# Performance work log

Hardware: AMD Instinct MI355X
Metric: run time of the kernel (lower is better)

Reference implementation:

```python
import jax, jax.numpy as jnp
import numpy as np

D_MODEL = 1024
NHEAD = 16
HEAD_DIM = D_MODEL // NHEAD
B, T = 4, 2048


def setup_inputs() -> dict:
    key = jax.random.key(0)
    ks = jax.random.split(key, 5)
    s = 0.02
    return {
        "x": jax.random.normal(ks[0], (B, T, D_MODEL), dtype=jnp.float32),
        "w_qkv": jax.random.normal(ks[1], (D_MODEL, 3 * D_MODEL), dtype=jnp.float32) * s,
        "b_qkv": jnp.zeros((3 * D_MODEL,), dtype=jnp.float32),
        "w_proj": jax.random.normal(ks[2], (D_MODEL, D_MODEL), dtype=jnp.float32) * s,
        "b_proj": jnp.zeros((D_MODEL,), dtype=jnp.float32),
    }


def reference(x, w_qkv, b_qkv, w_proj, b_proj):
    Bx, Tx, D = x.shape
    qkv = x @ w_qkv + b_qkv                      # [B,T,3D]
    qkv = qkv.reshape(Bx, Tx, 3, NHEAD, HEAD_DIM)
    q, k, v = qkv[:, :, 0], qkv[:, :, 1], qkv[:, :, 2]   # [B,T,H,hd]
    q = q.transpose(0, 2, 1, 3)                  # [B,H,T,hd]
    k = k.transpose(0, 2, 1, 3)
    v = v.transpose(0, 2, 1, 3)
    scale = 1.0 / jnp.sqrt(jnp.asarray(HEAD_DIM, dtype=x.dtype))
    attn = jnp.einsum("bhqd,bhkd->bhqk", q, k) * scale   # [B,H,T,T]
    causal = jnp.tril(jnp.ones((Tx, Tx), dtype=bool))
    attn = jnp.where(causal[None, None], attn, jnp.asarray(-jnp.inf, dtype=attn.dtype))
    attn = jax.nn.softmax(attn, axis=-1)
    # dropout p=0.0 (eval / identity)
    out = jnp.einsum("bhqk,bhkd->bhqd", attn, v)          # [B,H,T,hd]
    out = out.transpose(0, 2, 1, 3).reshape(Bx, Tx, D)
    return out @ w_proj + b_proj
```

## Files before the change

### kernel.cpp

```cpp
#include <hip/hip_runtime.h>
#include <hip/hip_bf16.h>
#include <math.h>

#define D_MODEL 1024
#define NH      16
#define HD      64
#define T_SEQ   2048
#define B_SZ    4
#define M_ROWS  (B_SZ * T_SEQ)
#define N_QKV   (3 * D_MODEL)

typedef __bf16 bf16x8 __attribute__((ext_vector_type(8)));
typedef __bf16 bf16x4 __attribute__((ext_vector_type(4)));
typedef float  f32x4  __attribute__((ext_vector_type(4)));

__device__ __forceinline__ bf16x8 cvt8(float4 a, float4 b) {
    bf16x8 v;
    v[0]=(__bf16)a.x; v[1]=(__bf16)a.y; v[2]=(__bf16)a.z; v[3]=(__bf16)a.w;
    v[4]=(__bf16)b.x; v[5]=(__bf16)b.y; v[6]=(__bf16)b.z; v[7]=(__bf16)b.w;
    return v;
}

__device__ __forceinline__ void gload_lds16(const __bf16* g, __bf16* l) {
    __builtin_amdgcn_global_load_lds(
        (const __attribute__((address_space(1))) void*)g,
        (__attribute__((address_space(3))) void*)l, 16, 0, 0);
}

__global__ __launch_bounds__(256) void cvt_bf16(const float* __restrict__ in,
                                                __bf16* __restrict__ out, int n8)
{
    int i = blockIdx.x * 256 + threadIdx.x;
    if (i < n8) {
        float4 a = ((const float4*)in)[2 * i];
        float4 b = ((const float4*)in)[2 * i + 1];
        ((bf16x8*)out)[i] = cvt8(a, b);
    }
}

__global__ __launch_bounds__(256) void transpose_cvt(
    const float* __restrict__ W, __bf16* __restrict__ WT, int R, int C)
{
    __shared__ float t[32][33];
    const int tr0 = blockIdx.y * 32, tc0 = blockIdx.x * 32;
    const int lr = threadIdx.x >> 5, lc = threadIdx.x & 31;
    #pragma unroll
    for (int i = 0; i < 4; ++i)
        t[lr + i * 8][lc] = W[(size_t)(tr0 + lr + i * 8) * C + tc0 + lc];
    __syncthreads();
    #pragma unroll
    for (int i = 0; i < 4; ++i)
        WT[(size_t)(tc0 + lr + i * 8) * R + tr0 + lc] = (__bf16)t[lc][lr + i * 8];
}

template<int MODE>
__global__ __launch_bounds__(256) void gemm_mfma(
    const __bf16* __restrict__ A, const __bf16* __restrict__ BT,
    const float* __restrict__ bias, void* __restrict__ C0,
    __bf16* __restrict__ vT, int M, int N, int K)
{
    __shared__ __bf16 As[128 * 32];
    __shared__ __bf16 Bs[128 * 32];

    const int nbn = N >> 7;
    const int nwg = gridDim.x;
    int bid = blockIdx.x;
    bid = (bid & 7) * (nwg >> 3) + (bid >> 3);
    const int tm = bid / nbn, tn = bid % nbn;
    const int row0 = tm << 7, col0 = tn << 7;

    const int tid  = threadIdx.x;
    const int wid  = tid >> 6, lane = tid & 63;
    const int wm   = wid >> 1, wn = wid & 1;
    const int g    = lane >> 4, r16 = lane & 15;

    const int srow = lane >> 2;
    const int skk  = (lane & 3) * 8;

    f32x4 acc[4][4] = {};

    for (int k0 = 0; k0 < K; k0 += 32) {
        #pragma unroll
        for (int i = 0; i < 2; ++i) {
            const int seg = wid * 2 + i;
            const int row = seg * 16 + srow;
            gload_lds16(A  + (size_t)(row0 + row) * K + k0 + skk, As + seg * 512);
            gload_lds16(BT + (size_t)(col0 + row) * K + k0 + skk, Bs + seg * 512);
        }
        __syncthreads();

        bf16x8 af[4], bfr[4];
        #pragma unroll
        for (int mt = 0; mt < 4; ++mt)
            af[mt] = *(const bf16x8*)&As[(wm * 64 + mt * 16 + r16) * 32 + g * 8];
        #pragma unroll
        for (int nt = 0; nt < 4; ++nt)
            bfr[nt] = *(const bf16x8*)&Bs[(wn * 64 + nt * 16 + r16) * 32 + g * 8];
        #pragma unroll
        for (int mt = 0; mt < 4; ++mt)
            #pragma unroll
            for (int nt = 0; nt < 4; ++nt)
                acc[mt][nt] = __builtin_amdgcn_mfma_f32_16x16x32_bf16(
                    af[mt], bfr[nt], acc[mt][nt], 0, 0, 0);
        __syncthreads();
    }

    const bool isV = (MODE == 1) && (tn >= 16);

    #pragma unroll
    for (int mt = 0; mt < 4; ++mt) {
        #pragma unroll
        for (int nt = 0; nt < 4; ++nt) {
            const int col = col0 + wn * 64 + nt * 16 + r16;
            const float bv = bias[col];
            const int rowb = row0 + wm * 64 + mt * 16 + g * 4;
            if (MODE == 0) {
                #pragma unroll
                for (int j = 0; j < 4; ++j)
                    ((float*)C0)[(size_t)(rowb + j) * N + col] = acc[mt][nt][j] + bv;
            } else if (!isV) {
                #pragma unroll
                for (int j = 0; j < 4; ++j)
                    ((__bf16*)C0)[(size_t)(rowb + j) * 2048 + col] =
                        (__bf16)(acc[mt][nt][j] + bv);
            } else {
                const int hh = (col - 2048) >> 6, dd = (col - 2048) & 63;
                const int bb = rowb >> 11, tt = rowb & 2047;
                __bf16 p4[4];
                #pragma unroll
                for (int j = 0; j < 4; ++j) p4[j] = (__bf16)(acc[mt][nt][j] + bv);
                *(bf16x4*)&vT[((size_t)((bb * NH + hh) * HD + dd)) * T_SEQ + tt]
                    = *(const bf16x4*)p4;
            }
        }
    }
}

__global__ __launch_bounds__(256) void attn_mfma(
    const __bf16* __restrict__ qkb, const __bf16* __restrict__ vT,
    __bf16* __restrict__ aout)
{
    const int idx = blockIdx.x;
    const int qt  = 15 - (idx >> 6);
    const int bh  = idx & 63;
    const int b   = bh >> 4;
    const int h   = bh & 15;
    const int tid  = threadIdx.x;
    const int wid  = tid >> 6;
    const int lane = tid & 63;
    const int g    = lane >> 4;
    const int n    = lane & 15;
    const int swzn = (n & 7) << 4;

    const int q0    = qt * 128;
    const int qbase = q0 + wid * 32;
    const int nkt   = 2 * qt + 2;

    __shared__ __align__(16) char Ks[64 * 128];
    __shared__ __align__(16) char Vs[64 * 128];
    __shared__ __align__(16) char Ps[4][32 * 128];

    const int srow = tid >> 2;
    const int sb0  = (tid & 3) << 4;
    const int swzw = (srow & 7) << 4;
    const int sd8  = (tid & 3) * 8;

    bf16x8 qa[2][2];
    #pragma unroll
    for (int rb = 0; rb < 2; ++rb) {
        const size_t qrow = (size_t)(b * T_SEQ + qbase + rb * 16 + n) * 2048
                            + (size_t)h * HD;
        qa[rb][0] = *(const bf16x8*)&qkb[qrow + g * 8];
        qa[rb][1] = *(const bf16x8*)&qkb[qrow + 32 + g * 8];
        #pragma unroll
        for (int j = 0; j < 8; ++j) {
            qa[rb][0][j] = (__bf16)((float)qa[rb][0][j] * 0.125f);
            qa[rb][1][j] = (__bf16)((float)qa[rb][1][j] * 0.125f);
        }
    }

    f32x4 o[2][4] = {};
    float mrow[2][4] = {};
    float lrow[2][4] = {};

    const __bf16* gK = qkb + (size_t)(b * T_SEQ + srow) * 2048 + 1024
                       + (size_t)h * HD + sd8;
    const __bf16* gV = vT + ((size_t)((b * NH + h) * HD + srow)) * T_SEQ + sd8;

    bf16x8 kreg0 = *(const bf16x8*)gK;
    bf16x8 kreg1 = *(const bf16x8*)(gK + 32);
    bf16x8 vreg0 = *(const bf16x8*)gV;
    bf16x8 vreg1 = *(const bf16x8*)(gV + 32);

    for (int kt = 0; kt < nkt; ++kt) {
        *(bf16x8*)(Ks + srow * 128 + (sb0 ^ swzw))        = kreg0;
        *(bf16x8*)(Ks + srow * 128 + ((sb0 + 64) ^ swzw)) = kreg1;
        *(bf16x8*)(Vs + srow * 128 + (sb0 ^ swzw))        = vreg0;
        *(bf16x8*)(Vs + srow * 128 + ((sb0 + 64) ^ swzw)) = vreg1;
        __syncthreads();

        if (kt + 1 < nkt) {
            const size_t kb2 = (size_t)(kt + 1) * 64;
            kreg0 = *(const bf16x8*)(gK + kb2 * 2048);
            kreg1 = *(const bf16x8*)(gK + kb2 * 2048 + 32);
            vreg0 = *(const bf16x8*)(gV + kb2);
            vreg1 = *(const bf16x8*)(gV + kb2 + 32);
        }

        f32x4 s4[2][4] = {};
        __builtin_amdgcn_s_setprio(1);
        #pragma unroll
        for (int cc = 0; cc < 2; ++cc) {
            bf16x8 kf[4];
            #pragma unroll
            for (int sub = 0; sub < 4; ++sub)
                kf[sub] = *(const bf16x8*)(Ks + (sub * 16 + n) * 128
                                           + ((cc * 64 + g * 16) ^ swzn));
            #pragma unroll
            for (int rb = 0; rb < 2; ++rb)
                #pragma unroll
                for (int sub = 0; sub < 4; ++sub)
                    s4[rb][sub] = __builtin_amdgcn_mfma_f32_16x16x32_bf16(
                        qa[rb][cc], kf[sub], s4[rb][sub], 0, 0, 0);
        }
        __builtin_amdgcn_s_setprio(0);

        const int kb0 = kt * 64;
        const bool needmask = (kb0 + 63 > qbase);

        #pragma unroll
        for (int rb = 0; rb < 2; ++rb) {
            if (needmask) {
                #pragma unroll
                for (int r = 0; r < 4; ++r) {
                    const int qrow = qbase + rb * 16 + 4 * g + r;
                    #pragma unroll
                    for (int sub = 0; sub < 4; ++sub)
                        if (kb0 + sub * 16 + n > qrow) s4[rb][sub][r] = -INFINITY;
                }
            }
            float pm[4];
            int ok = 1;
            #pragma unroll
            for (int r = 0; r < 4; ++r) {
                pm[r] = fmaxf(fmaxf(s4[rb][0][r], s4[rb][1][r]),
                              fmaxf(s4[rb][2][r], s4[rb][3][r]));
                ok &= (pm[r] <= mrow[rb][r] + 8.f);
            }
            if (__all(ok)) {
                #pragma unroll
                for (int r = 0; r < 4; ++r) {
                    const float m = mrow[rb][r];
                    const float p0 = __expf(s4[rb][0][r] - m);
                    const float p1 = __expf(s4[rb][1][r] - m);
                    const float p2 = __expf(s4[rb][2][r] - m);
                    const float p3 = __expf(s4[rb][3][r] - m);
                    lrow[rb][r] += (p0 + p1) + (p2 + p3);
                    char* prow = Ps[wid] + (rb * 16 + 4 * g + r) * 128;
                    const int pswz = ((4 * g + r) & 7) << 4;
                    *(__bf16*)(prow + ((2 * n)      ^ pswz)) = (__bf16)p0;
                    *(__bf16*)(prow + ((2 * n + 32) ^ pswz)) = (__bf16)p1;
                    *(__bf16*)(prow + ((2 * n + 64) ^ pswz)) = (__bf16)p2;
                    *(__bf16*)(prow + ((2 * n + 96) ^ pswz)) = (__bf16)p3;
                }
            } else {
                #pragma unroll
                for (int r = 0; r < 4; ++r) {
                    float tm = pm[r];
                    #pragma unroll
                    for (int off = 1; off < 16; off <<= 1)
                        tm = fmaxf(tm, __shfl_xor(tm, off));
                    const float mnew = fmaxf(mrow[rb][r], tm);
                    const float corr = __expf(mrow[rb][r] - mnew);
                    mrow[rb][r] = mnew;
                    const float p0 = __expf(s4[rb][0][r] - mnew);
                    const float p1 = __expf(s4[rb][1][r] - mnew);
                    const float p2 = __expf(s4[rb][2][r] - mnew);
                    const float p3 = __expf(s4[rb][3][r] - mnew);
                    lrow[rb][r] = lrow[rb][r] * corr + (p0 + p1) + (p2 + p3);
                    #pragma unroll
                    for (int nt = 0; nt < 4; ++nt) o[rb][nt][r] *= corr;
                    char* prow = Ps[wid] + (rb * 16 + 4 * g + r) * 128;
                    const int pswz = ((4 * g + r) & 7) << 4;
                    *(__bf16*)(prow + ((2 * n)      ^ pswz)) = (__bf16)p0;
                    *(__bf16*)(prow + ((2 * n + 32) ^ pswz)) = (__bf16)p1;
                    *(__bf16*)(prow + ((2 * n + 64) ^ pswz)) = (__bf16)p2;
                    *(__bf16*)(prow + ((2 * n + 96) ^ pswz)) = (__bf16)p3;
                }
            }
        }

        __builtin_amdgcn_s_setprio(1);
        #pragma unroll
        for (int cc = 0; cc < 2; ++cc) {
            bf16x8 vf[4];
            #pragma unroll
            for (int nt = 0; nt < 4; ++nt)
                vf[nt] = *(const bf16x8*)(Vs + (nt * 16 + n) * 128
                                          + ((cc * 64 + g * 16) ^ swzn));
            #pragma unroll
            for (int rb = 0; rb < 2; ++rb) {
                bf16x8 pa = *(const bf16x8*)(Ps[wid] + (rb * 16 + n) * 128
                                             + ((cc * 64 + g * 16) ^ swzn));
                #pragma unroll
                for (int nt = 0; nt < 4; ++nt)
                    o[rb][nt] = __builtin_amdgcn_mfma_f32_16x16x32_bf16(
                        pa, vf[nt], o[rb][nt], 0, 0, 0);
            }
        }
        __builtin_amdgcn_s_setprio(0);
        __syncthreads();
    }

    #pragma unroll
    for (int rb = 0; rb < 2; ++rb) {
        float inv[4];
        #pragma unroll
        for (int r = 0; r < 4; ++r) {
            float s = lrow[rb][r];
            #pragma unroll
            for (int off = 1; off < 16; off <<= 1)
                s += __shfl_xor(s, off);
            inv[r] = 1.f / s;
        }
        const size_t obase = (size_t)(b * T_SEQ + qbase + rb * 16) * D_MODEL
                             + (size_t)h * HD;
        #pragma unroll
        for (int nt = 0; nt < 4; ++nt)
            #pragma unroll
            for (int r = 0; r < 4; ++r)
                aout[obase + (size_t)(4 * g + r) * D_MODEL + nt * 16 + n]
                    = (__bf16)(o[rb][nt][r] * inv[r]);
    }
}

extern "C" void kernel_launch(void* const* d_in, const int* in_sizes, int n_in,
                              void* d_out, int out_size, void* d_ws, size_t ws_size,
                              hipStream_t stream)
{
    const float* x      = (const float*)d_in[0];
    const float* w_qkv  = (const float*)d_in[1];
    const float* b_qkv  = (const float*)d_in[2];
    const float* w_proj = (const float*)d_in[3];
    const float* b_proj = (const float*)d_in[4];
    float* out = (float*)d_out;

    char* ws = (char*)d_ws;
    __bf16* qkb    = (__bf16*)ws;
    __bf16* vTb    = qkb + (size_t)M_ROWS * 2048;
    __bf16* xb     = vTb + (size_t)NH * B_SZ * HD * T_SEQ;
    __bf16* wqkvT  = xb + (size_t)M_ROWS * D_MODEL;
    __bf16* wprojT = wqkvT + (size_t)N_QKV * D_MODEL;
    __bf16* aout   = wprojT + (size_t)D_MODEL * D_MODEL;

    cvt_bf16<<<dim3(M_ROWS * D_MODEL / 8 / 256), 256, 0, stream>>>(
        x, xb, M_ROWS * D_MODEL / 8);
    transpose_cvt<<<dim3(N_QKV / 32, D_MODEL / 32), 256, 0, stream>>>(
        w_qkv, wqkvT, D_MODEL, N_QKV);
    transpose_cvt<<<dim3(D_MODEL / 32, D_MODEL / 32), 256, 0, stream>>>(
        w_proj, wprojT, D_MODEL, D_MODEL);

    gemm_mfma<1><<<dim3((M_ROWS / 128) * (N_QKV / 128)), 256, 0, stream>>>(
        xb, wqkvT, b_qkv, qkb, vTb, M_ROWS, N_QKV, D_MODEL);

    attn_mfma<<<dim3(B_SZ * NH * 16), 256, 0, stream>>>(qkb, vTb, aout);

    gemm_mfma<0><<<dim3((M_ROWS / 128) * (D_MODEL / 128)), 256, 0, stream>>>(
        aout, wprojT, b_proj, out, nullptr, M_ROWS, D_MODEL, D_MODEL);
}
```

Measured before the change: 209.5 us.

## Double GEMM K-tile with XOR-swizzled LDS and use exp2 in attention softmax

The GEMM K-step grows from 32 to 64, halving the number of barrier pairs per tile. LDS rows are XOR-swizzled so fragment reads avoid bank conflicts. In attention, log2(e) is folded into the Q scale and __expf is replaced by a raw v_exp_f32, removing a multiply per exponential. The margin-8 skip test now works in base-2 units, which changes when the rescale path triggers. LDS per GEMM block also doubles.

```diff
diff --git a/kernel.cpp b/kernel.cpp
--- a/kernel.cpp
+++ b/kernel.cpp
@@ -27,6 +27,12 @@
         (__attribute__((address_space(3))) void*)l, 16, 0, 0);
 }
 
+__device__ __forceinline__ float exp2v(float x) {
+    float r;
+    asm("v_exp_f32 %0, %1" : "=v"(r) : "v"(x));
+    return r;
+}
+
 __global__ __launch_bounds__(256) void cvt_bf16(const float* __restrict__ in,
                                                 __bf16* __restrict__ out, int n8)
 {
@@ -59,8 +65,8 @@
     const float* __restrict__ bias, void* __restrict__ C0,
     __bf16* __restrict__ vT, int M, int N, int K)
 {
-    __shared__ __bf16 As[128 * 32];
-    __shared__ __bf16 Bs[128 * 32];
+    __shared__ __bf16 As[128 * 64];
+    __shared__ __bf16 Bs[128 * 64];
 
     const int nbn = N >> 7;
     const int nwg = gridDim.x;
@@ -74,34 +80,41 @@
     const int wm   = wid >> 1, wn = wid & 1;
     const int g    = lane >> 4, r16 = lane & 15;
 
-    const int srow = lane >> 2;
-    const int skk  = (lane & 3) * 8;
-
     f32x4 acc[4][4] = {};
 
-    for (int k0 = 0; k0 < K; k0 += 32) {
-        #pragma unroll
-        for (int i = 0; i < 2; ++i) {
-            const int seg = wid * 2 + i;
-            const int row = seg * 16 + srow;
-            gload_lds16(A  + (size_t)(row0 + row) * K + k0 + skk, As + seg * 512);
-            gload_lds16(BT + (size_t)(col0 + row) * K + k0 + skk, Bs + seg * 512);
+    for (int k0 = 0; k0 < K; k0 += 64) {
+        #pragma unroll
+        for (int i = 0; i < 4; ++i) {
+            const int seg = wid * 4 + i;
+            const int row = seg * 8 + (lane >> 3);
+            const int kel = ((lane & 7) * 8) ^ ((row & 7) * 8);
+            gload_lds16(A  + (size_t)(row0 + row) * K + k0 + kel, As + seg * 512);
+            gload_lds16(BT + (size_t)(col0 + row) * K + k0 + kel, Bs + seg * 512);
         }
         __syncthreads();
 
-        bf16x8 af[4], bfr[4];
-        #pragma unroll
-        for (int mt = 0; mt < 4; ++mt)
-            af[mt] = *(const bf16x8*)&As[(wm * 64 + mt * 16 + r16) * 32 + g * 8];
-        #pragma unroll
-        for (int nt = 0; nt < 4; ++nt)
-            bfr[nt] = *(const bf16x8*)&Bs[(wn * 64 + nt * 16 + r16) * 32 + g * 8];
-        #pragma unroll
-        for (int mt = 0; mt < 4; ++mt)
-            #pragma unroll
-            for (int nt = 0; nt < 4; ++nt)
-                acc[mt][nt] = __builtin_amdgcn_mfma_f32_16x16x32_bf16(
-                    af[mt], bfr[nt], acc[mt][nt], 0, 0, 0);
+        #pragma unroll
+        for (int kk = 0; kk < 2; ++kk) {
+            bf16x8 af[4], bfr[4];
+            #pragma unroll
+            for (int mt = 0; mt < 4; ++mt) {
+                const int row = wm * 64 + mt * 16 + r16;
+                af[mt] = *(const bf16x8*)((const char*)As + row * 128
+                             + ((kk * 64 + g * 16) ^ ((row & 7) << 4)));
+            }
+            #pragma unroll
+            for (int nt = 0; nt < 4; ++nt) {
+                const int row = wn * 64 + nt * 16 + r16;
+                bfr[nt] = *(const bf16x8*)((const char*)Bs + row * 128
+                             + ((kk * 64 + g * 16) ^ ((row & 7) << 4)));
+            }
+            #pragma unroll
+            for (int mt = 0; mt < 4; ++mt)
+                #pragma unroll
+                for (int nt = 0; nt < 4; ++nt)
+                    acc[mt][nt] = __builtin_amdgcn_mfma_f32_16x16x32_bf16(
+                        af[mt], bfr[nt], acc[mt][nt], 0, 0, 0);
+        }
         __syncthreads();
     }
 
@@ -165,6 +178,7 @@
     const int swzw = (srow & 7) << 4;
     const int sd8  = (tid & 3) * 8;
 
+    const float qscale = 0.125f * 1.44269504089f;
     bf16x8 qa[2][2];
     #pragma unroll
     for (int rb = 0; rb < 2; ++rb) {
@@ -174,8 +188,8 @@
         qa[rb][1] = *(const bf16x8*)&qkb[qrow + 32 + g * 8];
         #pragma unroll
         for (int j = 0; j < 8; ++j) {
-            qa[rb][0][j] = (__bf16)((float)qa[rb][0][j] * 0.125f);
-            qa[rb][1][j] = (__bf16)((float)qa[rb][1][j] * 0.125f);
+            qa[rb][0][j] = (__bf16)((float)qa[rb][0][j] * qscale);
+            qa[rb][1][j] = (__bf16)((float)qa[rb][1][j] * qscale);
         }
     }
 
@@ -251,10 +265,10 @@
                 #pragma unroll
                 for (int r = 0; r < 4; ++r) {
                     const float m = mrow[rb][r];
-                    const float p0 = __expf(s4[rb][0][r] - m);
-                    const float p1 = __expf(s4[rb][1][r] - m);
-                    const float p2 = __expf(s4[rb][2][r] - m);
-                    const float p3 = __expf(s4[rb][3][r] - m);
+                    const float p0 = exp2v(s4[rb][0][r] - m);
+                    const float p1 = exp2v(s4[rb][1][r] - m);
+                    const float p2 = exp2v(s4[rb][2][r] - m);
+                    const float p3 = exp2v(s4[rb][3][r] - m);
                     lrow[rb][r] += (p0 + p1) + (p2 + p3);
                     char* prow = Ps[wid] + (rb * 16 + 4 * g + r) * 128;
                     const int pswz = ((4 * g + r) & 7) << 4;
@@ -271,12 +285,12 @@
                     for (int off = 1; off < 16; off <<= 1)
                         tm = fmaxf(tm, __shfl_xor(tm, off));
                     const float mnew = fmaxf(mrow[rb][r], tm);
-                    const float corr = __expf(mrow[rb][r] - mnew);
+                    const float corr = exp2v(mrow[rb][r] - mnew);
                     mrow[rb][r] = mnew;
-                    const float p0 = __expf(s4[rb][0][r] - mnew);
-                    const float p1 = __expf(s4[rb][1][r] - mnew);
-                    const float p2 = __expf(s4[rb][2][r] - mnew);
-                    const float p3 = __expf(s4[rb][3][r] - mnew);
+                    const float p0 = exp2v(s4[rb][0][r] - mnew);
+                    const float p1 = exp2v(s4[rb][1][r] - mnew);
+                    const float p2 = exp2v(s4[rb][2][r] - mnew);
+                    const float p3 = exp2v(s4[rb][3][r] - mnew);
                     lrow[rb][r] = lrow[rb][r] * corr + (p0 + p1) + (p2 + p3);
                     #pragma unroll
                     for (int nt = 0; nt < 4; ++nt) o[rb][nt][r] *= corr;
```

New measurement: 195.4 us. 1.07x faster.
